# Performance work log

Hardware: AMD Instinct MI355X
Metric: run time of the kernel (lower is better)

## Reference

```python
import jax, jax.numpy as jnp
import numpy as np

DILATIONS = (1, 3, 6, 12)          # layer dilations, flattened from [[1,3],[6,12]]
BLOCKS = ((0, 1), (2, 3))           # block -> layer indices
H_SIZE = 32
STATE_SIZE = 128
OUT_SIZE = STATE_SIZE - H_SIZE      # 96
INPUT_SIZE = 64
OUTPUT_SIZE = 64
T, B = 512, 512


def _linear_params(k, fan_in, fan_out):
    bound = 1.0 / np.sqrt(fan_in)
    kw, kb = jax.random.split(k)
    W = jax.random.uniform(kw, (fan_out, fan_in), minval=-bound, maxval=bound, dtype=jnp.float32)
    b = jax.random.uniform(kb, (fan_out,), minval=-bound, maxval=bound, dtype=jnp.float32)
    return W, b


def setup_inputs() -> dict:
    key = jax.random.key(0)
    ks = jax.random.split(key, 8)
    x = jax.random.normal(ks[0], (T, B, INPUT_SIZE), dtype=jnp.float32)
    ins = [INPUT_SIZE, OUT_SIZE, OUT_SIZE, OUT_SIZE]  # first layer sees raw input
    out = {"x": x}
    for l in range(4):
        W, b = _linear_params(ks[1 + l], ins[l] + 2 * H_SIZE, 4 * STATE_SIZE)
        out[f"W{l}"] = W
        out[f"b{l}"] = b
    Wa, ba = _linear_params(ks[5], OUT_SIZE, OUTPUT_SIZE)
    out["Wa"] = Wa
    out["ba"] = ba
    return out


def _s2cell(W, b, inp, prev_h, second_h, prev_c, delayed_c, has_prev, has_del):
    # xh = cat(input, prev_h, delayed_h-or-prev_h) ; zeros when no prev state (handled by caller masks)
    xh = jnp.concatenate([inp, prev_h, second_h], axis=1)
    g = xh @ W.T + b                                     # [B, 4*state]
    g0, g1, g2, g3 = jnp.split(g, 4, axis=1)
    forget = jax.nn.sigmoid(g0 + 1.0)
    cand = jnp.tanh(g1)
    alpha = jax.nn.sigmoid(g2)
    out_gate = jax.nn.sigmoid(g3)
    weighted = jnp.where(has_del, alpha * prev_c + (1.0 - alpha) * delayed_c, prev_c)
    new_c = jnp.where(has_prev, forget * weighted + (1.0 - forget) * cand, cand)
    whole = out_gate * new_c
    return whole[:, :OUT_SIZE], whole[:, OUT_SIZE:], new_c


def reference(x, W0, b0, W1, b1, W2, b2, W3, b3, Wa, ba):
    Ws = [W0, W1, W2, W3]
    bs = [b0, b1, b2, b3]
    batch = x.shape[1]
    h0 = tuple(jnp.zeros((d, batch, H_SIZE), jnp.float32) for d in DILATIONS)
    c0 = tuple(jnp.zeros((d, batch, STATE_SIZE), jnp.float32) for d in DILATIONS)

    def step(carry, inp_t):
        t, h_bufs, c_bufs = carry
        h_bufs = list(h_bufs)
        c_bufs = list(c_bufs)
        has_prev = t >= 1
        prev_block = None
        out_t = None
        for iblock, layers in enumerate(BLOCKS):
            for j, l in enumerate(layers):
                cur_in = (inp_t if iblock == 0 else prev_block) if j == 0 else out_t
                d = DILATIONS[l]
                # ring buffer: slot (t-1)%d holds state at t-1, slot t%d still holds state at t-d
                prev_h = jnp.where(has_prev, h_bufs[l][(t - 1) % d], 0.0)
                prev_c = c_bufs[l][(t - 1) % d]
                has_del = t >= d
                del_h = jnp.where(has_del, h_bufs[l][t % d], prev_h)
                del_c = c_bufs[l][t % d]
                out_t, new_h, new_c = _s2cell(Ws[l], bs[l], cur_in, prev_h, del_h,
                                              prev_c, del_c, has_prev, has_del)
                h_bufs[l] = h_bufs[l].at[t % d].set(new_h)
                c_bufs[l] = c_bufs[l].at[t % d].set(new_c)
            prev_block = out_t if iblock == 0 else out_t + prev_block  # resnet shortcut
        y = prev_block @ Wa.T + ba
        return (t + 1, tuple(h_bufs), tuple(c_bufs)), y

    _, ys = jax.lax.scan(step, (jnp.int32(0), h0, c0), x)
    return ys  # [T, B, output_size]
```

## Files before the change

### kernel.cpp

```cpp
#include <hip/hip_runtime.h>

typedef unsigned int uint;
typedef unsigned short ushort;
typedef unsigned long long u64;
typedef __attribute__((ext_vector_type(8))) short bf16x8;
typedef __attribute__((ext_vector_type(4))) float f32x4;
typedef __attribute__((ext_vector_type(4))) uint u32x4;

#define T_STEPS 512
#define BATCH   512
#define NB      8
#define RD      16
#define XSF     164
#define SSZ     128
#define OUTC    96
#define HC      32

__device__ __forceinline__ ushort f2bf(float f){
  uint u = __builtin_bit_cast(uint, f);
  u = (u + 0x7FFFu + ((u >> 16) & 1u)) >> 16;
  return (ushort)u;
}
__device__ __forceinline__ float bf2f(ushort h){
  uint u = ((uint)h) << 16; return __builtin_bit_cast(float, u);
}
__device__ __forceinline__ float sigm(float x){
  float e = __builtin_exp2f(-1.44269504f * x);
  return __builtin_amdgcn_rcpf(1.0f + e);
}
__device__ __forceinline__ float tanh_fast(float x){
  float e = __builtin_exp2f(-2.88539008f * x);
  return 2.0f * __builtin_amdgcn_rcpf(1.0f + e) - 1.0f;
}
__device__ __forceinline__ uint aload32(const uint* p){
  return __hip_atomic_load(p, __ATOMIC_RELAXED, __HIP_MEMORY_SCOPE_AGENT);
}
__device__ __forceinline__ void astore32(uint* p, uint v){
  __hip_atomic_store(p, v, __ATOMIC_RELAXED, __HIP_MEMORY_SCOPE_AGENT);
}
__device__ __forceinline__ u64 aload64(const u64* p){
  return __hip_atomic_load(p, __ATOMIC_RELAXED, __HIP_MEMORY_SCOPE_AGENT);
}
__device__ __forceinline__ void astore64(u64* p, u64 v){
  __hip_atomic_store(p, v, __ATOMIC_RELAXED, __HIP_MEMORY_SCOPE_AGENT);
}
__device__ __forceinline__ uint cvtpk(float a, float b){
  uint r; asm("v_cvt_pk_bf16_f32 %0, %1, %2" : "=v"(r) : "v"(a), "v"(b)); return r;
}
__device__ __forceinline__ void mk_frag(const float* p, bf16x8& ahi, bf16x8& alo){
  f32x4 a0 = *(const f32x4*)(p);
  f32x4 a1 = *(const f32x4*)(p + 4);
  u32x4 hw, lw;
  hw[0] = cvtpk(a0[0], a0[1]);
  hw[1] = cvtpk(a0[2], a0[3]);
  hw[2] = cvtpk(a1[0], a1[1]);
  hw[3] = cvtpk(a1[2], a1[3]);
  float r0 = a0[0] - __builtin_bit_cast(float, hw[0] << 16);
  float r1 = a0[1] - __builtin_bit_cast(float, hw[0] & 0xffff0000u);
  float r2 = a0[2] - __builtin_bit_cast(float, hw[1] << 16);
  float r3 = a0[3] - __builtin_bit_cast(float, hw[1] & 0xffff0000u);
  float r4 = a1[0] - __builtin_bit_cast(float, hw[2] << 16);
  float r5 = a1[1] - __builtin_bit_cast(float, hw[2] & 0xffff0000u);
  float r6 = a1[2] - __builtin_bit_cast(float, hw[3] << 16);
  float r7 = a1[3] - __builtin_bit_cast(float, hw[3] & 0xffff0000u);
  lw[0] = cvtpk(r0, r1);
  lw[1] = cvtpk(r2, r3);
  lw[2] = cvtpk(r4, r5);
  lw[3] = cvtpk(r6, r7);
  ahi = __builtin_bit_cast(bf16x8, hw);
  alo = __builtin_bit_cast(bf16x8, lw);
}

__global__ __launch_bounds__(512, 2)
void rnn_pipeline(const float* __restrict__ x,
                  const float* __restrict__ W0, const float* __restrict__ b0,
                  const float* __restrict__ W1, const float* __restrict__ b1,
                  const float* __restrict__ W2, const float* __restrict__ b2,
                  const float* __restrict__ W3, const float* __restrict__ b3,
                  const float* __restrict__ Wa, const float* __restrict__ ba,
                  float* __restrict__ y_out,
                  uint* __restrict__ prod, uint* __restrict__ consA,
                  uint* __restrict__ consB,
                  float* __restrict__ hop0, float* __restrict__ hop1,
                  float* __restrict__ hop2)
{
  const int tid  = threadIdx.x;
  const int wv   = tid >> 6;
  const int lane = tid & 63;
  const int l15  = lane & 15;
  const int hi   = lane >> 4;
  const int rep  = blockIdx.x & 63;
  const int stage= blockIdx.x >> 6;
  const int b0r  = rep * NB;

  const int dil = (stage==0)?1:(stage==1)?3:(stage==2)?6:12;
  const int KIN = (stage==0)?64:96;
  const int K   = KIN + 64;
  const float* Wl = (stage==0)?W0:(stage==1)?W1:(stage==2)?W2:W3;
  const float* bl = (stage==0)?b0:(stage==1)?b1:(stage==2)?b2:b3;

  __shared__ __align__(16) float sh_xh[16*XSF];
  __shared__ __align__(16) float sh_c[12*SSZ*NB + 16];
  __shared__ __align__(16) float sh_h[12*NB*HC];
  __shared__ __align__(16) float sh_out[NB*OUTC];
  __shared__ __align__(16) float sh_o1[NB*OUTC];

  for (int i = tid; i < 16*XSF; i += 512) sh_xh[i] = 0.0f;
  for (int i = tid; i < 12*SSZ*NB + 16; i += 512) sh_c[i] = 0.0f;
  for (int i = tid; i < 12*NB*HC; i += 512) sh_h[i] = 0.0f;
  for (int i = tid; i < NB*OUTC; i += 512) { sh_out[i] = 0.0f; sh_o1[i] = 0.0f; }

  const int sidx = 16*wv + l15;

  bf16x8 whi[4][5], wlo[4][5];
  #pragma unroll
  for (int j = 0; j < 4; ++j){
    const int grow = 128*j + sidx;
    #pragma unroll
    for (int ks = 0; ks < 5; ++ks){
      bf16x8 vh, vl;
      const int cb = ks*32 + hi*8;
      if (cb < K){
        const float* p = Wl + (size_t)grow*K + cb;
        #pragma unroll
        for (int i = 0; i < 8; ++i){
          float w = p[i];
          ushort h = f2bf(w);
          vh[i] = (short)h;
          vl[i] = (short)f2bf(w - bf2f(h));
        }
      } else {
        #pragma unroll
        for (int i = 0; i < 8; ++i){ vh[i] = 0; vl[i] = 0; }
      }
      whi[j][ks] = vh; wlo[j][ks] = vl;
    }
  }
  float bias[4];
  #pragma unroll
  for (int j = 0; j < 4; ++j) bias[j] = bl[128*j + sidx];

  bf16x8 phi[3], plo[3];
  #pragma unroll
  for (int ks = 0; ks < 3; ++ks){
    bf16x8 z;
    #pragma unroll
    for (int i = 0; i < 8; ++i) z[i]=0;
    phi[ks]=z; plo[ks]=z;
  }
  float bav = 0.0f;
  if (stage == 3 && wv < 4){
    const int ocol = 16*wv + l15;
    #pragma unroll
    for (int ks = 0; ks < 3; ++ks){
      const float* p = Wa + (size_t)ocol*96 + ks*32 + hi*8;
      bf16x8 vh, vl;
      #pragma unroll
      for (int i = 0; i < 8; ++i){
        float w = p[i];
        ushort h = f2bf(w);
        vh[i] = (short)h;
        vl[i] = (short)f2bf(w - bf2f(h));
      }
      phi[ks] = vh; plo[ks] = vl;
    }
    bav = ba[ocol];
  }

  uint* up_prod = (stage>0)? &prod[(stage-1)*64 + rep] : nullptr;
  uint* my_prod = (stage<3)? &prod[stage*64 + rep]     : nullptr;
  uint* dnA     = (stage<3)? &consA[stage*64 + rep]    : nullptr;
  uint* dnB     = (stage==1)? &consB[rep] : nullptr;
  const float* hop_in  = (stage==1)?hop0:(stage==2)?hop1:(stage==3)?hop2:nullptr;
  float*       hop_out = (stage==0)?hop0:(stage==1)?hop1:(stage==2)?hop2:nullptr;

  __syncthreads();

  int cur = 0, prv = dil - 1;
  for (int t = 0; t < T_STEPS; ++t){
    const int slot = t & (RD-1);
    if (lane == 0){
      if (stage > 0){
        while (aload32(up_prod) < (uint)(t+1)) __builtin_amdgcn_s_sleep(2);
      }
      if (stage < 3 && t >= RD){
        const uint need = (uint)(t - RD + 1);
        while (aload32(dnA) < need) __builtin_amdgcn_s_sleep(2);
        if (stage == 1){
          while (aload32(dnB) < need) __builtin_amdgcn_s_sleep(2);
        }
      }
    }

    if (stage == 0){
      const int r = tid >> 6, c = tid & 63;
      sh_xh[r*XSF + c] = x[(size_t)(t*BATCH + b0r + r)*64 + c];
    } else if (stage < 3){
      if (tid < 384){
        u64 v = aload64((const u64*)(hop_in + (size_t)(slot*64 + rep)*768) + tid);
        const int f = 2*tid, r = f/96, c = f%96;
        sh_xh[r*XSF + c]     = __builtin_bit_cast(float, (uint)(v & 0xffffffffull));
        sh_xh[r*XSF + c + 1] = __builtin_bit_cast(float, (uint)(v >> 32));
      }
    } else {
      const u64* src2 = (const u64*)(hop2 + (size_t)(slot*64 + rep)*768);
      const u64* src1 = (const u64*)(hop1 + (size_t)(slot*64 + rep)*768);
      for (int j = tid; j < 768; j += 512){
        if (j < 384){
          u64 v = aload64(src2 + j);
          const int f = 2*j, r = f/96, c = f%96;
          sh_xh[r*XSF + c]     = __builtin_bit_cast(float, (uint)(v & 0xffffffffull));
          sh_xh[r*XSF + c + 1] = __builtin_bit_cast(float, (uint)(v >> 32));
        } else {
          const int k = j - 384;
          u64 v = aload64(src1 + k);
          sh_o1[2*k]     = __builtin_bit_cast(float, (uint)(v & 0xffffffffull));
          sh_o1[2*k + 1] = __builtin_bit_cast(float, (uint)(v >> 32));
        }
      }
    }
    {
      const int which = tid >> 8, rem = tid & 255, r = rem >> 5, c = rem & 31;
      const float vp = sh_h[prv*(NB*HC) + r*HC + c];
      float val = vp;
      if (which == 1) val = (t >= dil) ? sh_h[cur*(NB*HC) + r*HC + c] : vp;
      sh_xh[r*XSF + KIN + which*32 + c] = val;
    }
    __syncthreads();
    if (tid == 0){
      if (stage == 1) astore32(&consA[0*64 + rep], (uint)(t+1));
      else if (stage == 2) astore32(&consA[1*64 + rep], (uint)(t+1));
      else if (stage == 3){ astore32(&consA[2*64 + rep], (uint)(t+1));
                            astore32(&consB[rep], (uint)(t+1)); }
    }

    f32x4 acc[4];
    #pragma unroll
    for (int j = 0; j < 4; ++j) acc[j] = (f32x4){bias[j],bias[j],bias[j],bias[j]};
    const float* arow = sh_xh + l15*XSF;
    #pragma unroll
    for (int ks = 0; ks < 5; ++ks){
      bf16x8 ahi, alo;
      mk_frag(arow + ks*32 + hi*8, ahi, alo);
      #pragma unroll
      for (int j = 0; j < 4; ++j){
        acc[j] = __builtin_amdgcn_mfma_f32_16x16x32_bf16(ahi, whi[j][ks], acc[j], 0, 0, 0);
        acc[j] = __builtin_amdgcn_mfma_f32_16x16x32_bf16(alo, whi[j][ks], acc[j], 0, 0, 0);
        acc[j] = __builtin_amdgcn_mfma_f32_16x16x32_bf16(ahi, wlo[j][ks], acc[j], 0, 0, 0);
      }
    }

    f32x4 pc = *(const f32x4*)(sh_c + prv*(SSZ*NB) + sidx*NB + hi*4);
    f32x4 dc = *(const f32x4*)(sh_c + cur*(SSZ*NB) + sidx*NB + hi*4);
    const bool has_prev = (t >= 1), has_del = (t >= dil);
    f32x4 ncv; float whv[4];
    #pragma unroll
    for (int k = 0; k < 4; ++k){
      float f  = sigm(acc[0][k] + 1.0f);
      float cd = tanh_fast(acc[1][k]);
      float al = sigm(acc[2][k]);
      float og = sigm(acc[3][k]);
      float wt = has_del ? (al*pc[k] + (1.0f - al)*dc[k]) : pc[k];
      float nc = has_prev ? (f*wt + (1.0f - f)*cd) : cd;
      ncv[k] = nc;
      whv[k] = og * nc;
    }
    if (hi < 2){
      *(f32x4*)(sh_c + cur*(SSZ*NB) + sidx*NB + hi*4) = ncv;
      #pragma unroll
      for (int k = 0; k < 4; ++k){
        const int r = hi*4 + k;
        if (sidx < OUTC) sh_out[r*OUTC + sidx] = whv[k];
        else             sh_h[cur*(NB*HC) + r*HC + (sidx - OUTC)] = whv[k];
      }
    }
    __syncthreads();

    if (stage < 3){
      if (tid < 384){
        u64 v = *(const u64*)(sh_out + 2*tid);
        astore64((u64*)(hop_out + (size_t)(slot*64 + rep)*768) + tid, v);
      }
      asm volatile("s_waitcnt vmcnt(0)" ::: "memory");
      __syncthreads();
      if (tid == 0) astore32(my_prod, (uint)(t+1));
    } else {
      for (int j = tid; j < 768; j += 512){
        const int r = j / 96, c = j % 96;
        sh_xh[r*XSF + c] = sh_out[j] + sh_o1[j];
      }
      __syncthreads();
      if (wv < 4){
        f32x4 acc1 = (f32x4){bav, bav, bav, bav};
        const float* prow = sh_xh + l15*XSF;
        #pragma unroll
        for (int ks = 0; ks < 3; ++ks){
          bf16x8 ahi, alo;
          mk_frag(prow + ks*32 + hi*8, ahi, alo);
          acc1 = __builtin_amdgcn_mfma_f32_16x16x32_bf16(ahi, phi[ks], acc1, 0, 0, 0);
          acc1 = __builtin_amdgcn_mfma_f32_16x16x32_bf16(alo, phi[ks], acc1, 0, 0, 0);
          acc1 = __builtin_amdgcn_mfma_f32_16x16x32_bf16(ahi, plo[ks], acc1, 0, 0, 0);
        }
        if (hi < 2){
          const int ocol = 16*wv + l15;
          #pragma unroll
          for (int k = 0; k < 4; ++k){
            const int r = hi*4 + k;
            y_out[(size_t)(t*BATCH + b0r + r)*64 + ocol] = acc1[k];
          }
        }
      }
      __syncthreads();
    }
    prv = cur;
    cur = (cur + 1 == dil) ? 0 : cur + 1;
  }
}

extern "C" void kernel_launch(void* const* d_in, const int* in_sizes, int n_in,
                              void* d_out, int out_size, void* d_ws, size_t ws_size,
                              hipStream_t stream) {
  (void)in_sizes; (void)n_in; (void)out_size; (void)ws_size;
  const float* x  = (const float*)d_in[0];
  const float* W0 = (const float*)d_in[1];
  const float* b0 = (const float*)d_in[2];
  const float* W1 = (const float*)d_in[3];
  const float* b1 = (const float*)d_in[4];
  const float* W2 = (const float*)d_in[5];
  const float* b2 = (const float*)d_in[6];
  const float* W3 = (const float*)d_in[7];
  const float* b3 = (const float*)d_in[8];
  const float* Wa = (const float*)d_in[9];
  const float* ba = (const float*)d_in[10];
  float* out = (float*)d_out;

  uint* prod  = (uint*)d_ws;
  uint* consA = prod + 192;
  uint* consB = consA + 192;
  float* hop0 = (float*)((char*)d_ws + 4096);
  float* hop1 = hop0 + (size_t)RD*64*768;
  float* hop2 = hop1 + (size_t)RD*64*768;

  hipMemsetAsync(d_ws, 0, 4096, stream);
  hipLaunchKernelGGL(rnn_pipeline, dim3(256), dim3(512), 0, stream,
                     x, W0, b0, W1, b1, W2, b2, W3, b3, Wa, ba,
                     out, prod, consA, consB, hop0, hop1, hop2);
}
```

Baseline: 2.331 ms.

## Prefetch next-step inputs, pre-split bf16 hi/lo planes in LDS, defer producer flag

Activations are now stored in LDS and in the inter-stage hop buffers as precomputed bf16 hi/lo planes, so the per-step fp32-to-split conversion before the MFMAs goes away. The next timestep's input (x or the upstream hop data) is prefetched into registers during the current step's MFMA work. Producer flag publication is moved to the start of the next step, which drops one vmcnt wait and one barrier per step, and one trailing barrier in the last stage is removed. The costs are a more intricate flag protocol that is easy to get wrong, plus extra register pressure from the prefetch. The extra bf16 split of the residual sum on the hop path also costs some precision.

```diff
diff --git a/kernel.cpp b/kernel.cpp
--- a/kernel.cpp
+++ b/kernel.cpp
@@ -5,16 +5,14 @@
 typedef unsigned long long u64;
 typedef __attribute__((ext_vector_type(8))) short bf16x8;
 typedef __attribute__((ext_vector_type(4))) float f32x4;
-typedef __attribute__((ext_vector_type(4))) uint u32x4;
 
 #define T_STEPS 512
 #define BATCH   512
 #define NB      8
 #define RD      16
-#define XSF     164
-#define SSZ     128
+#define XS      168
+#define CSTR    12
 #define OUTC    96
-#define HC      32
 
 __device__ __forceinline__ ushort f2bf(float f){
   uint u = __builtin_bit_cast(uint, f);
@@ -43,32 +41,6 @@
 }
 __device__ __forceinline__ void astore64(u64* p, u64 v){
   __hip_atomic_store(p, v, __ATOMIC_RELAXED, __HIP_MEMORY_SCOPE_AGENT);
-}
-__device__ __forceinline__ uint cvtpk(float a, float b){
-  uint r; asm("v_cvt_pk_bf16_f32 %0, %1, %2" : "=v"(r) : "v"(a), "v"(b)); return r;
-}
-__device__ __forceinline__ void mk_frag(const float* p, bf16x8& ahi, bf16x8& alo){
-  f32x4 a0 = *(const f32x4*)(p);
-  f32x4 a1 = *(const f32x4*)(p + 4);
-  u32x4 hw, lw;
-  hw[0] = cvtpk(a0[0], a0[1]);
-  hw[1] = cvtpk(a0[2], a0[3]);
-  hw[2] = cvtpk(a1[0], a1[1]);
-  hw[3] = cvtpk(a1[2], a1[3]);
-  float r0 = a0[0] - __builtin_bit_cast(float, hw[0] << 16);
-  float r1 = a0[1] - __builtin_bit_cast(float, hw[0] & 0xffff0000u);
-  float r2 = a0[2] - __builtin_bit_cast(float, hw[1] << 16);
-  float r3 = a0[3] - __builtin_bit_cast(float, hw[1] & 0xffff0000u);
-  float r4 = a1[0] - __builtin_bit_cast(float, hw[2] << 16);
-  float r5 = a1[1] - __builtin_bit_cast(float, hw[2] & 0xffff0000u);
-  float r6 = a1[2] - __builtin_bit_cast(float, hw[3] << 16);
-  float r7 = a1[3] - __builtin_bit_cast(float, hw[3] & 0xffff0000u);
-  lw[0] = cvtpk(r0, r1);
-  lw[1] = cvtpk(r2, r3);
-  lw[2] = cvtpk(r4, r5);
-  lw[3] = cvtpk(r6, r7);
-  ahi = __builtin_bit_cast(bf16x8, hw);
-  alo = __builtin_bit_cast(bf16x8, lw);
 }
 
 __global__ __launch_bounds__(512, 2)
@@ -81,8 +53,8 @@
                   float* __restrict__ y_out,
                   uint* __restrict__ prod, uint* __restrict__ consA,
                   uint* __restrict__ consB,
-                  float* __restrict__ hop0, float* __restrict__ hop1,
-                  float* __restrict__ hop2)
+                  u64* __restrict__ hop0, u64* __restrict__ hop1,
+                  u64* __restrict__ hop2)
 {
   const int tid  = threadIdx.x;
   const int wv   = tid >> 6;
@@ -99,16 +71,19 @@
   const float* Wl = (stage==0)?W0:(stage==1)?W1:(stage==2)?W2:W3;
   const float* bl = (stage==0)?b0:(stage==1)?b1:(stage==2)?b2:b3;
 
-  __shared__ __align__(16) float sh_xh[16*XSF];
-  __shared__ __align__(16) float sh_c[12*SSZ*NB + 16];
-  __shared__ __align__(16) float sh_h[12*NB*HC];
-  __shared__ __align__(16) float sh_out[NB*OUTC];
-  __shared__ __align__(16) float sh_o1[NB*OUTC];
-
-  for (int i = tid; i < 16*XSF; i += 512) sh_xh[i] = 0.0f;
-  for (int i = tid; i < 12*SSZ*NB + 16; i += 512) sh_c[i] = 0.0f;
-  for (int i = tid; i < 12*NB*HC; i += 512) sh_h[i] = 0.0f;
-  for (int i = tid; i < NB*OUTC; i += 512) { sh_out[i] = 0.0f; sh_o1[i] = 0.0f; }
+  __shared__ __align__(16) ushort xh_hi[16*XS], xh_lo[16*XS];
+  __shared__ __align__(16) float  sh_c[12*128*CSTR];
+  __shared__ __align__(16) ushort h_hi[12*NB*32], h_lo[12*NB*32];
+  __shared__ __align__(16) ushort outp[2304];
+  __shared__ __align__(16) ushort o1p[1536];
+  __shared__ __align__(16) float  o3f[NB*OUTC];
+
+  for (int i = tid; i < 16*XS; i += 512){ xh_hi[i] = 0; xh_lo[i] = 0; }
+  for (int i = tid; i < 12*128*CSTR; i += 512) sh_c[i] = 0.0f;
+  for (int i = tid; i < 12*NB*32; i += 512){ h_hi[i] = 0; h_lo[i] = 0; }
+  for (int i = tid; i < 2304; i += 512) outp[i] = 0;
+  for (int i = tid; i < 1536; i += 512) o1p[i] = 0;
+  for (int i = tid; i < NB*OUTC; i += 512) o3f[i] = 0.0f;
 
   const int sidx = 16*wv + l15;
 
@@ -167,91 +142,124 @@
     bav = ba[ocol];
   }
 
-  uint* up_prod = (stage>0)? &prod[(stage-1)*64 + rep] : nullptr;
-  uint* my_prod = (stage<3)? &prod[stage*64 + rep]     : nullptr;
-  uint* dnA     = (stage<3)? &consA[stage*64 + rep]    : nullptr;
-  uint* dnB     = (stage==1)? &consB[rep] : nullptr;
-  const float* hop_in  = (stage==1)?hop0:(stage==2)?hop1:(stage==3)?hop2:nullptr;
-  float*       hop_out = (stage==0)?hop0:(stage==1)?hop1:(stage==2)?hop2:nullptr;
+  uint* up_prod  = (stage==1)? &prod[rep] : (stage==2)? &prod[64+rep] :
+                   (stage==3)? &prod[128+rep] : nullptr;
+  uint* up_prod1 = (stage==3)? &prod[64+rep] : nullptr;
+  uint* my_prod  = (stage==0)? &prod[rep] : (stage==1)? &prod[64+rep] :
+                   (stage==2)? &prod[128+rep] : nullptr;
+  uint* my_consA = (stage==1)? &consA[rep] : (stage==2)? &consA[64+rep] :
+                   (stage==3)? &consA[128+rep] : nullptr;
+  uint* my_consB = (stage==3)? &consB[rep] : nullptr;
+  uint* dnA      = (stage==0)? &consA[rep] : (stage==1)? &consA[64+rep] :
+                   (stage==2)? &consA[128+rep] : nullptr;
+  uint* dnB      = (stage==1)? &consB[rep] : nullptr;
+  const u64* hop_in  = (stage==1)? hop0 : (stage==2)? hop1 : nullptr;
+  u64*       hop_out = (stage==0)? hop0 : (stage==1)? hop1 : (stage==2)? hop2 : nullptr;
 
   __syncthreads();
+
+  u64 pfA = 0, pfB = 0; float xv = 0.0f;
+  if (stage == 0){
+    const int r = tid >> 6, c = tid & 63;
+    xv = x[(size_t)(b0r + r)*64 + c];
+  } else if (stage < 3){
+    uint f = aload32(up_prod);
+    while (f < 1u){ __builtin_amdgcn_s_sleep(2); f = aload32(up_prod); }
+    if (tid < 384) pfA = aload64(hop_in + (size_t)rep*384 + tid);
+  } else {
+    uint f = aload32(up_prod);
+    while (f < 1u){ __builtin_amdgcn_s_sleep(2); f = aload32(up_prod); }
+    f = aload32(up_prod1);
+    while (f < 1u){ __builtin_amdgcn_s_sleep(2); f = aload32(up_prod1); }
+    const u64* s2 = hop2 + (size_t)rep*384;
+    const u64* s1 = hop1 + (size_t)rep*384;
+    pfA = (tid < 384) ? aload64(s2 + tid) : aload64(s1 + (tid - 384));
+    if (tid < 256) pfB = aload64(s1 + 128 + tid);
+  }
 
   int cur = 0, prv = dil - 1;
   for (int t = 0; t < T_STEPS; ++t){
     const int slot = t & (RD-1);
-    if (lane == 0){
-      if (stage > 0){
-        while (aload32(up_prod) < (uint)(t+1)) __builtin_amdgcn_s_sleep(2);
-      }
-      if (stage < 3 && t >= RD){
-        const uint need = (uint)(t - RD + 1);
-        while (aload32(dnA) < need) __builtin_amdgcn_s_sleep(2);
-        if (stage == 1){
-          while (aload32(dnB) < need) __builtin_amdgcn_s_sleep(2);
-        }
-      }
-    }
-
+
+    asm volatile("s_waitcnt vmcnt(0)" ::: "memory");
     if (stage == 0){
       const int r = tid >> 6, c = tid & 63;
-      sh_xh[r*XSF + c] = x[(size_t)(t*BATCH + b0r + r)*64 + c];
-    } else if (stage < 3){
+      ushort hb = f2bf(xv);
+      xh_hi[r*XS + c] = hb;
+      xh_lo[r*XS + c] = f2bf(xv - bf2f(hb));
+    } else {
       if (tid < 384){
-        u64 v = aload64((const u64*)(hop_in + (size_t)(slot*64 + rep)*768) + tid);
-        const int f = 2*tid, r = f/96, c = f%96;
-        sh_xh[r*XSF + c]     = __builtin_bit_cast(float, (uint)(v & 0xffffffffull));
-        sh_xh[r*XSF + c + 1] = __builtin_bit_cast(float, (uint)(v >> 32));
-      }
-    } else {
-      const u64* src2 = (const u64*)(hop2 + (size_t)(slot*64 + rep)*768);
-      const u64* src1 = (const u64*)(hop1 + (size_t)(slot*64 + rep)*768);
-      for (int j = tid; j < 768; j += 512){
-        if (j < 384){
-          u64 v = aload64(src2 + j);
-          const int f = 2*j, r = f/96, c = f%96;
-          sh_xh[r*XSF + c]     = __builtin_bit_cast(float, (uint)(v & 0xffffffffull));
-          sh_xh[r*XSF + c + 1] = __builtin_bit_cast(float, (uint)(v >> 32));
-        } else {
-          const int k = j - 384;
-          u64 v = aload64(src1 + k);
-          sh_o1[2*k]     = __builtin_bit_cast(float, (uint)(v & 0xffffffffull));
-          sh_o1[2*k + 1] = __builtin_bit_cast(float, (uint)(v >> 32));
-        }
-      }
+        const int q = (tid < 192) ? tid : tid - 192;
+        ushort* plane = (tid < 192) ? xh_hi : xh_lo;
+        const int r = q / 24, c4 = (q % 24) * 4;
+        *(u64*)(plane + r*XS + c4) = pfA;
+      } else if (stage == 3){
+        *(u64*)(o1p + 4*(tid - 384)) = pfA;
+      }
+      if (stage == 3 && tid < 256) *(u64*)(o1p + 4*(128 + tid)) = pfB;
     }
     {
       const int which = tid >> 8, rem = tid & 255, r = rem >> 5, c = rem & 31;
-      const float vp = sh_h[prv*(NB*HC) + r*HC + c];
-      float val = vp;
-      if (which == 1) val = (t >= dil) ? sh_h[cur*(NB*HC) + r*HC + c] : vp;
-      sh_xh[r*XSF + KIN + which*32 + c] = val;
+      const int srcslot = (which == 1 && t >= dil) ? cur : prv;
+      xh_hi[r*XS + KIN + which*32 + c] = h_hi[srcslot*(NB*32) + r*32 + c];
+      xh_lo[r*XS + KIN + which*32 + c] = h_lo[srcslot*(NB*32) + r*32 + c];
     }
     __syncthreads();
     if (tid == 0){
-      if (stage == 1) astore32(&consA[0*64 + rep], (uint)(t+1));
-      else if (stage == 2) astore32(&consA[1*64 + rep], (uint)(t+1));
-      else if (stage == 3){ astore32(&consA[2*64 + rep], (uint)(t+1));
-                            astore32(&consB[rep], (uint)(t+1)); }
-    }
+      if (stage > 0){
+        astore32(my_consA, (uint)(t+1));
+        if (stage == 3) astore32(my_consB, (uint)(t+1));
+      }
+      if (stage < 3 && t > 0) astore32(my_prod, (uint)t);
+    }
+    const bool pre = (t + 1 < T_STEPS);
+    uint up_f = 0, up_f1 = 0, dn_f = 0, dn_fB = 0;
+    if (pre && stage > 0)  up_f  = aload32(up_prod);
+    if (pre && stage == 3) up_f1 = aload32(up_prod1);
+    if (stage < 3)         dn_f  = aload32(dnA);
+    if (stage == 1)        dn_fB = aload32(dnB);
 
     f32x4 acc[4];
     #pragma unroll
     for (int j = 0; j < 4; ++j) acc[j] = (f32x4){bias[j],bias[j],bias[j],bias[j]};
-    const float* arow = sh_xh + l15*XSF;
+    const int abase = l15*XS + hi*8;
     #pragma unroll
     for (int ks = 0; ks < 5; ++ks){
-      bf16x8 ahi, alo;
-      mk_frag(arow + ks*32 + hi*8, ahi, alo);
-      #pragma unroll
-      for (int j = 0; j < 4; ++j){
-        acc[j] = __builtin_amdgcn_mfma_f32_16x16x32_bf16(ahi, whi[j][ks], acc[j], 0, 0, 0);
-        acc[j] = __builtin_amdgcn_mfma_f32_16x16x32_bf16(alo, whi[j][ks], acc[j], 0, 0, 0);
-        acc[j] = __builtin_amdgcn_mfma_f32_16x16x32_bf16(ahi, wlo[j][ks], acc[j], 0, 0, 0);
-      }
-    }
-
-    f32x4 pc = *(const f32x4*)(sh_c + prv*(SSZ*NB) + sidx*NB + hi*4);
-    f32x4 dc = *(const f32x4*)(sh_c + cur*(SSZ*NB) + sidx*NB + hi*4);
+      if (ks*32 < K){
+        bf16x8 ahi = *(const bf16x8*)(xh_hi + abase + ks*32);
+        bf16x8 alo = *(const bf16x8*)(xh_lo + abase + ks*32);
+        #pragma unroll
+        for (int j = 0; j < 4; ++j){
+          acc[j] = __builtin_amdgcn_mfma_f32_16x16x32_bf16(ahi, whi[j][ks], acc[j], 0, 0, 0);
+          acc[j] = __builtin_amdgcn_mfma_f32_16x16x32_bf16(alo, whi[j][ks], acc[j], 0, 0, 0);
+          acc[j] = __builtin_amdgcn_mfma_f32_16x16x32_bf16(ahi, wlo[j][ks], acc[j], 0, 0, 0);
+        }
+      }
+    }
+
+    if (pre){
+      if (stage == 0){
+        const int r = tid >> 6, c = tid & 63;
+        xv = x[(size_t)((t+1)*BATCH + b0r + r)*64 + c];
+      } else {
+        const uint need = (uint)(t + 2);
+        while (up_f < need){ __builtin_amdgcn_s_sleep(2); up_f = aload32(up_prod); }
+        if (stage == 3)
+          while (up_f1 < need){ __builtin_amdgcn_s_sleep(2); up_f1 = aload32(up_prod1); }
+        const int ns = (t + 1) & (RD-1);
+        if (stage < 3){
+          if (tid < 384) pfA = aload64(hop_in + (size_t)(ns*64 + rep)*384 + tid);
+        } else {
+          const u64* s2 = hop2 + (size_t)(ns*64 + rep)*384;
+          const u64* s1 = hop1 + (size_t)(ns*64 + rep)*384;
+          pfA = (tid < 384) ? aload64(s2 + tid) : aload64(s1 + (tid - 384));
+          if (tid < 256) pfB = aload64(s1 + 128 + tid);
+        }
+      }
+    }
+
+    f32x4 pc = *(const f32x4*)(sh_c + prv*(128*CSTR) + sidx*CSTR + hi*4);
+    f32x4 dc = *(const f32x4*)(sh_c + cur*(128*CSTR) + sidx*CSTR + hi*4);
     const bool has_prev = (t >= 1), has_del = (t >= dil);
     f32x4 ncv; float whv[4];
     #pragma unroll
@@ -266,37 +274,54 @@
       whv[k] = og * nc;
     }
     if (hi < 2){
-      *(f32x4*)(sh_c + cur*(SSZ*NB) + sidx*NB + hi*4) = ncv;
+      *(f32x4*)(sh_c + cur*(128*CSTR) + sidx*CSTR + hi*4) = ncv;
       #pragma unroll
       for (int k = 0; k < 4; ++k){
         const int r = hi*4 + k;
-        if (sidx < OUTC) sh_out[r*OUTC + sidx] = whv[k];
-        else             sh_h[cur*(NB*HC) + r*HC + (sidx - OUTC)] = whv[k];
+        const float w = whv[k];
+        if (sidx < OUTC){
+          if (stage == 3){
+            o3f[r*OUTC + sidx] = w;
+          } else {
+            ushort hb = f2bf(w);
+            outp[r*OUTC + sidx]       = hb;
+            outp[768 + r*OUTC + sidx] = f2bf(w - bf2f(hb));
+          }
+        } else {
+          ushort hb = f2bf(w);
+          h_hi[cur*(NB*32) + r*32 + (sidx - OUTC)] = hb;
+          h_lo[cur*(NB*32) + r*32 + (sidx - OUTC)] = f2bf(w - bf2f(hb));
+        }
       }
     }
     __syncthreads();
 
     if (stage < 3){
+      if (t >= RD){
+        const uint need = (uint)(t - RD + 1);
+        while (dn_f < need){ __builtin_amdgcn_s_sleep(2); dn_f = aload32(dnA); }
+        if (stage == 1)
+          while (dn_fB < need){ __builtin_amdgcn_s_sleep(2); dn_fB = aload32(dnB); }
+      }
       if (tid < 384){
-        u64 v = *(const u64*)(sh_out + 2*tid);
-        astore64((u64*)(hop_out + (size_t)(slot*64 + rep)*768) + tid, v);
-      }
-      asm volatile("s_waitcnt vmcnt(0)" ::: "memory");
-      __syncthreads();
-      if (tid == 0) astore32(my_prod, (uint)(t+1));
+        u64 v = *(const u64*)(outp + 4*tid);
+        astore64(hop_out + (size_t)(slot*64 + rep)*384 + tid, v);
+      }
     } else {
       for (int j = tid; j < 768; j += 512){
-        const int r = j / 96, c = j % 96;
-        sh_xh[r*XSF + c] = sh_out[j] + sh_o1[j];
+        float v = o3f[j] + bf2f(o1p[j]) + bf2f(o1p[768 + j]);
+        ushort hb = f2bf(v);
+        outp[j]       = hb;
+        outp[768 + j] = f2bf(v - bf2f(hb));
       }
       __syncthreads();
       if (wv < 4){
         f32x4 acc1 = (f32x4){bav, bav, bav, bav};
-        const float* prow = sh_xh + l15*XSF;
+        const int pbase = l15*96 + hi*8;
         #pragma unroll
         for (int ks = 0; ks < 3; ++ks){
-          bf16x8 ahi, alo;
-          mk_frag(prow + ks*32 + hi*8, ahi, alo);
+          bf16x8 ahi = *(const bf16x8*)(outp + pbase + ks*32);
+          bf16x8 alo = *(const bf16x8*)(outp + 768 + pbase + ks*32);
           acc1 = __builtin_amdgcn_mfma_f32_16x16x32_bf16(ahi, phi[ks], acc1, 0, 0, 0);
           acc1 = __builtin_amdgcn_mfma_f32_16x16x32_bf16(alo, phi[ks], acc1, 0, 0, 0);
           acc1 = __builtin_amdgcn_mfma_f32_16x16x32_bf16(ahi, plo[ks], acc1, 0, 0, 0);
@@ -310,11 +335,14 @@
           }
         }
       }
-      __syncthreads();
     }
     prv = cur;
     cur = (cur + 1 == dil) ? 0 : cur + 1;
   }
+
+  asm volatile("s_waitcnt vmcnt(0)" ::: "memory");
+  __syncthreads();
+  if (stage < 3 && tid == 0) astore32(my_prod, (uint)(T_STEPS + 2));
 }
 
 extern "C" void kernel_launch(void* const* d_in, const int* in_sizes, int n_in,
@@ -337,9 +365,9 @@
   uint* prod  = (uint*)d_ws;
   uint* consA = prod + 192;
   uint* consB = consA + 192;
-  float* hop0 = (float*)((char*)d_ws + 4096);
-  float* hop1 = hop0 + (size_t)RD*64*768;
-  float* hop2 = hop1 + (size_t)RD*64*768;
+  u64* hop0 = (u64*)((char*)d_ws + 4096);
+  u64* hop1 = hop0 + (size_t)RD*64*384;
+  u64* hop2 = hop1 + (size_t)RD*64*384;
 
   hipMemsetAsync(d_ws, 0, 4096, stream);
   hipLaunchKernelGGL(rnn_pipeline, dim3(256), dim3(512), 0, stream,
```

New measurement: 2.708 ms. +16.1%, slower.
